# Optimization experiments

Hardware: AMD Instinct MI355X
Metric: run time of the kernel (lower is better)

## Reference

```python
import jax, jax.numpy as jnp
import numpy as np

N_NODES = 100000
N_EDGES = 1000000
IN_FEAT = 64
OUT_FEAT = 64


def setup_inputs() -> dict:
    key = jax.random.key(0)
    ks = jax.random.split(key, 12)
    d, o = IN_FEAT, OUT_FEAT
    s = 1.0 / np.sqrt(d)
    s2 = 1.0 / np.sqrt(2 * d)
    return {
        "x": jax.random.normal(ks[0], (N_NODES, d), dtype=jnp.float32),
        "edge_index": jax.random.randint(ks[1], (2, N_EDGES), 0, N_NODES, dtype=jnp.int64),
        "batch": jnp.zeros((N_NODES,), dtype=jnp.int64),
        # message MLP: Linear(d,d) -> ReLU -> Linear(d,d)
        "msg_w1": jax.random.uniform(ks[2], (d, d), jnp.float32, -s, s),
        "msg_b1": jax.random.uniform(ks[3], (d,), jnp.float32, -s, s),
        "msg_w2": jax.random.uniform(ks[4], (d, d), jnp.float32, -s, s),
        "msg_b2": jax.random.uniform(ks[5], (d,), jnp.float32, -s, s),
        # output MLP: Linear(2d,d) -> ReLU -> Linear(d,out)
        "out_w1": jax.random.uniform(ks[6], (2 * d, d), jnp.float32, -s2, s2),
        "out_b1": jax.random.uniform(ks[7], (d,), jnp.float32, -s2, s2),
        "out_w2": jax.random.uniform(ks[8], (d, o), jnp.float32, -s, s),
        "out_b2": jax.random.uniform(ks[9], (o,), jnp.float32, -s, s),
    }


def reference(x, edge_index, batch, msg_w1, msg_b1, msg_w2, msg_b2,
              out_w1, out_b1, out_w2, out_b2):
    row, col = edge_index[0], edge_index[1]
    # gather source-node features per edge, apply message MLP
    h = x[row]                                   # [E, d]
    msg = jax.nn.relu(h @ msg_w1 + msg_b1) @ msg_w2 + msg_b2  # [E, d]
    # force processor: node features pass through as fx; scatter-sum messages
    fx = x                                        # [N, d]
    agg = jax.ops.segment_sum(msg, col, num_segments=N_NODES)  # [N, d]
    out_final = jnp.concatenate([fx, agg], axis=1)  # [N, 2d]
    out = jax.nn.relu(out_final @ out_w1 + out_b1) @ out_w2 + out_b2  # [N, out]
    return out
```

## Files before the change

### kernel.cpp

```cpp
#include <hip/hip_runtime.h>
#include <hip/hip_bf16.h>

#define D 64
#define BSHIFT 7
#define BW (1 << BSHIFT)
#define MAXB 1024
#define CAP 8192
#define STRIDE 4096

typedef __attribute__((ext_vector_type(8))) short bf16x8;
typedef __attribute__((ext_vector_type(4))) float f32x4;

__device__ __forceinline__ short f2bf(float f) {
    __hip_bfloat16 h = __float2bfloat16(f);
    return *reinterpret_cast<short*>(&h);
}

__global__ __launch_bounds__(256) void msg_kernel(
    const float* __restrict__ x,
    const float* __restrict__ w1, const float* __restrict__ b1,
    const float* __restrict__ w2, const float* __restrict__ b2,
    __hip_bfloat16* __restrict__ m, int n_nodes)
{
    __shared__ __align__(16) __hip_bfloat16 sH[4][16 * 72];

    const int lane = threadIdx.x & 63;
    const int wslot = threadIdx.x >> 6;
    const int mr   = lane & 15;
    const int quad = lane >> 4;

    bf16x8 w1f[2][4], w2f[2][4];
    float  b1v[4], b2v[4];
#pragma unroll
    for (int ks = 0; ks < 2; ++ks)
#pragma unroll
        for (int nb = 0; nb < 4; ++nb) {
            bf16x8 f1, f2;
#pragma unroll
            for (int j = 0; j < 8; ++j) {
                int k = ks * 32 + quad * 8 + j;
                f1[j] = f2bf(w1[k * D + nb * 16 + mr]);
                f2[j] = f2bf(w2[k * D + nb * 16 + mr]);
            }
            w1f[ks][nb] = f1;
            w2f[ks][nb] = f2;
        }
#pragma unroll
    for (int nb = 0; nb < 4; ++nb) {
        b1v[nb] = b1[nb * 16 + mr];
        b2v[nb] = b2[nb * 16 + mr];
    }

    __hip_bfloat16* Hw = sH[wslot];
    const int wid    = (blockIdx.x * blockDim.x + threadIdx.x) >> 6;
    const int nwaves = (gridDim.x * blockDim.x) >> 6;
    const int ntiles = (n_nodes + 15) >> 4;

    for (int t = wid; t < ntiles; t += nwaves) {
        const int v0 = t * 16;
        int vr = v0 + mr;
        if (vr >= n_nodes) vr = n_nodes - 1;

        bf16x8 a[2];
#pragma unroll
        for (int ks = 0; ks < 2; ++ks) {
            const float* p = x + (size_t)vr * D + ks * 32 + quad * 8;
            float4 lo = *(const float4*)p;
            float4 hi = *(const float4*)(p + 4);
            bf16x8 f;
            f[0] = f2bf(lo.x); f[1] = f2bf(lo.y); f[2] = f2bf(lo.z); f[3] = f2bf(lo.w);
            f[4] = f2bf(hi.x); f[5] = f2bf(hi.y); f[6] = f2bf(hi.z); f[7] = f2bf(hi.w);
            a[ks] = f;
        }

#pragma unroll
        for (int nb = 0; nb < 4; ++nb) {
            f32x4 acc = {0.f, 0.f, 0.f, 0.f};
            acc = __builtin_amdgcn_mfma_f32_16x16x32_bf16(a[0], w1f[0][nb], acc, 0, 0, 0);
            acc = __builtin_amdgcn_mfma_f32_16x16x32_bf16(a[1], w1f[1][nb], acc, 0, 0, 0);
#pragma unroll
            for (int r = 0; r < 4; ++r) {
                float hv = fmaxf(acc[r] + b1v[nb], 0.f);
                Hw[(quad * 4 + r) * 72 + nb * 16 + mr] = __float2bfloat16(hv);
            }
        }

        bf16x8 h[2];
#pragma unroll
        for (int ks = 0; ks < 2; ++ks)
            h[ks] = *(const bf16x8*)&Hw[mr * 72 + ks * 32 + quad * 8];

#pragma unroll
        for (int nb = 0; nb < 4; ++nb) {
            f32x4 acc = {0.f, 0.f, 0.f, 0.f};
            acc = __builtin_amdgcn_mfma_f32_16x16x32_bf16(h[0], w2f[0][nb], acc, 0, 0, 0);
            acc = __builtin_amdgcn_mfma_f32_16x16x32_bf16(h[1], w2f[1][nb], acc, 0, 0, 0);
#pragma unroll
            for (int r = 0; r < 4; ++r)
                Hw[(quad * 4 + r) * 72 + nb * 16 + mr] =
                    __float2bfloat16(acc[r] + b2v[nb]);
        }

#pragma unroll
        for (int s = 0; s < 2; ++s) {
            const int rrow = s * 8 + (lane >> 3);
            const int cblk = (lane & 7) * 8;
            bf16x8 val = *(const bf16x8*)&Hw[rrow * 72 + cblk];
            const int vrow = v0 + rrow;
            if (vrow < n_nodes)
                *(bf16x8*)&m[(size_t)vrow * D + cblk] = val;
        }
    }
}

__global__ __launch_bounds__(256) void bin_kernel(
    const int* __restrict__ row, const int* __restrict__ col,
    int* __restrict__ gcur, unsigned int* __restrict__ tmp,
    int n_edges, int nbuckets, int chunk)
{
    __shared__ int hist[MAXB], base[MAXB], lcur[MAXB];
    const int t = threadIdx.x;
    const int e0 = blockIdx.x * chunk;
    const int e1 = min(e0 + chunk, n_edges);

    for (int i = t; i < nbuckets; i += 256) hist[i] = 0;
    __syncthreads();
    for (int e = e0 + t; e < e1; e += 256)
        atomicAdd(&hist[col[e] >> BSHIFT], 1);
    __syncthreads();
    for (int i = t; i < nbuckets; i += 256) {
        base[i] = hist[i] ? atomicAdd(&gcur[i], hist[i]) : 0;
        lcur[i] = 0;
    }
    __syncthreads();
    for (int e = e0 + t; e < e1; e += 256) {
        int c = col[e];
        int b = c >> BSHIFT;
        int loc = base[b] + atomicAdd(&lcur[b], 1);
        if (loc < STRIDE) {
            unsigned int val = ((unsigned int)(c & (BW - 1)) << 17)
                             | (unsigned int)row[e];
            tmp[(size_t)b * STRIDE + loc] = val;
        }
    }
}

__global__ __launch_bounds__(1024) void bucket_gather_kernel(
    const int* __restrict__ gcur, const unsigned int* __restrict__ tmp,
    const __hip_bfloat16* __restrict__ m, __hip_bfloat16* __restrict__ agg,
    int n_nodes, int nbuckets)
{
    __shared__ unsigned int sorted[CAP];
    __shared__ int cnt[BW], off[BW], cur[BW];

    const int b    = blockIdx.x;
    const int t    = threadIdx.x;
    const int lane = t & 63;
    const int wv   = t >> 6;
    const int vbase = b << BSHIFT;
    const unsigned int* gtmp = tmp + (size_t)b * STRIDE;

    const int total = min(gcur[b], STRIDE);

    float acc[8];
#pragma unroll
    for (int i = 0; i < 8; ++i) acc[i] = 0.f;

    for (int r0 = 0; r0 < total; r0 += CAP) {
        const int r1 = min(r0 + CAP, total);

        if (t < BW) cnt[t] = 0;
        __syncthreads();

        for (int i = r0 + t; i < r1; i += 1024)
            atomicAdd(&cnt[gtmp[i] >> 17], 1);
        __syncthreads();

        if (t < BW) off[t] = cnt[t];
        __syncthreads();
        for (int d = 1; d < BW; d <<= 1) {
            int u = 0;
            if (t < BW && t >= d) u = off[t - d];
            __syncthreads();
            if (t < BW) off[t] += u;
            __syncthreads();
        }
        if (t < BW) {
            int e = off[t] - cnt[t];
            off[t] = e;
            cur[t] = e;
        }
        __syncthreads();

        for (int i = r0 + t; i < r1; i += 1024) {
            unsigned int u = gtmp[i];
            int pos = atomicAdd(&cur[u >> 17], 1);
            sorted[pos] = u;
        }
        __syncthreads();

#pragma unroll
        for (int i = 0; i < 8; ++i) {
            const int n  = wv + (i << 4);
            const int o0 = off[n];
            const int c  = cnt[n];
            float s = 0.f;
            for (int cs = 0; cs < c; cs += 64) {
                const int k = min(64, c - cs);
                unsigned int pv = 0;
                if (lane < k) pv = sorted[o0 + cs + lane];

                int j = 0;
                for (; j + 8 <= k; j += 8) {
                    unsigned int u[8];
                    float v[8];
#pragma unroll
                    for (int q = 0; q < 8; ++q)
                        u[q] = __builtin_amdgcn_readlane(pv, j + q);
#pragma unroll
                    for (int q = 0; q < 8; ++q)
                        v[q] = (float)m[(size_t)(u[q] & 0x1FFFFu) * D + lane];
#pragma unroll
                    for (int q = 0; q < 8; ++q)
                        s += v[q];
                }
                for (; j < k; ++j) {
                    unsigned int u = __builtin_amdgcn_readlane(pv, j);
                    s += (float)m[(size_t)(u & 0x1FFFFu) * D + lane];
                }
            }
            acc[i] += s;
        }
        __syncthreads();
    }

#pragma unroll
    for (int i = 0; i < 8; ++i) {
        const int v = vbase + wv + (i << 4);
        if (v < n_nodes)
            agg[(size_t)v * D + lane] = __float2bfloat16(acc[i]);
    }
}

__global__ __launch_bounds__(256) void scatter_kernel(
    const int* __restrict__ row, const int* __restrict__ col,
    const __hip_bfloat16* __restrict__ m, float* __restrict__ aggf, int n_edges)
{
    const int lane = threadIdx.x & 63;
    const int wid  = (blockIdx.x * blockDim.x + threadIdx.x) >> 6;
    const int base = wid * 64;
    if (base >= n_edges) return;
    const int cnt = min(64, n_edges - base);

    int my_r = 0, my_c = 0;
    if (lane < cnt) { my_r = row[base + lane]; my_c = col[base + lane]; }

    for (int j = 0; j < cnt; ++j) {
        int r = __builtin_amdgcn_readlane(my_r, j);
        int c = __builtin_amdgcn_readlane(my_c, j);
        float v = (float)m[(size_t)r * D + lane];
        atomicAdd(&aggf[(size_t)c * D + lane], v);
    }
}

__global__ __launch_bounds__(256) void cvt_kernel(
    const float* __restrict__ aggf, __hip_bfloat16* __restrict__ agg, int n)
{
    int i = blockIdx.x * blockDim.x + threadIdx.x;
    if (i < n) agg[i] = __float2bfloat16(aggf[i]);
}

__global__ __launch_bounds__(256) void out_kernel(
    const float* __restrict__ x, const __hip_bfloat16* __restrict__ agg,
    const float* __restrict__ w1, const float* __restrict__ b1,
    const float* __restrict__ w2, const float* __restrict__ b2,
    float* __restrict__ out, int n_nodes)
{
    __shared__ __align__(16) __hip_bfloat16 sH[4][16 * 72];

    const int lane = threadIdx.x & 63;
    const int wslot = threadIdx.x >> 6;
    const int mr   = lane & 15;
    const int quad = lane >> 4;

    bf16x8 w1f[4][4], w2f[2][4];
    float  b1v[4], b2v[4];
#pragma unroll
    for (int ks = 0; ks < 4; ++ks)
#pragma unroll
        for (int nb = 0; nb < 4; ++nb) {
            bf16x8 f;
#pragma unroll
            for (int j = 0; j < 8; ++j) {
                int k = ks * 32 + quad * 8 + j;
                f[j] = f2bf(w1[k * D + nb * 16 + mr]);
            }
            w1f[ks][nb] = f;
        }
#pragma unroll
    for (int ks = 0; ks < 2; ++ks)
#pragma unroll
        for (int nb = 0; nb < 4; ++nb) {
            bf16x8 f;
#pragma unroll
            for (int j = 0; j < 8; ++j) {
                int k = ks * 32 + quad * 8 + j;
                f[j] = f2bf(w2[k * D + nb * 16 + mr]);
            }
            w2f[ks][nb] = f;
        }
#pragma unroll
    for (int nb = 0; nb < 4; ++nb) {
        b1v[nb] = b1[nb * 16 + mr];
        b2v[nb] = b2[nb * 16 + mr];
    }

    __hip_bfloat16* Hw = sH[wslot];
    const int wid    = (blockIdx.x * blockDim.x + threadIdx.x) >> 6;
    const int nwaves = (gridDim.x * blockDim.x) >> 6;
    const int ntiles = (n_nodes + 15) >> 4;

    for (int t = wid; t < ntiles; t += nwaves) {
        const int v0 = t * 16;
        int vr = v0 + mr;
        if (vr >= n_nodes) vr = n_nodes - 1;

        bf16x8 a[4];
#pragma unroll
        for (int ks = 0; ks < 2; ++ks) {
            const float* p = x + (size_t)vr * D + ks * 32 + quad * 8;
            float4 lo = *(const float4*)p;
            float4 hi = *(const float4*)(p + 4);
            bf16x8 f;
            f[0] = f2bf(lo.x); f[1] = f2bf(lo.y); f[2] = f2bf(lo.z); f[3] = f2bf(lo.w);
            f[4] = f2bf(hi.x); f[5] = f2bf(hi.y); f[6] = f2bf(hi.z); f[7] = f2bf(hi.w);
            a[ks] = f;
        }
#pragma unroll
        for (int ks = 2; ks < 4; ++ks)
            a[ks] = *(const bf16x8*)&agg[(size_t)vr * D + (ks - 2) * 32 + quad * 8];

#pragma unroll
        for (int nb = 0; nb < 4; ++nb) {
            f32x4 acc = {0.f, 0.f, 0.f, 0.f};
#pragma unroll
            for (int ks = 0; ks < 4; ++ks)
                acc = __builtin_amdgcn_mfma_f32_16x16x32_bf16(a[ks], w1f[ks][nb], acc, 0, 0, 0);
#pragma unroll
            for (int r = 0; r < 4; ++r) {
                float hv = fmaxf(acc[r] + b1v[nb], 0.f);
                Hw[(quad * 4 + r) * 72 + nb * 16 + mr] = __float2bfloat16(hv);
            }
        }

        bf16x8 h[2];
#pragma unroll
        for (int ks = 0; ks < 2; ++ks)
            h[ks] = *(const bf16x8*)&Hw[mr * 72 + ks * 32 + quad * 8];

#pragma unroll
        for (int nb = 0; nb < 4; ++nb) {
            f32x4 acc = {0.f, 0.f, 0.f, 0.f};
            acc = __builtin_amdgcn_mfma_f32_16x16x32_bf16(h[0], w2f[0][nb], acc, 0, 0, 0);
            acc = __builtin_amdgcn_mfma_f32_16x16x32_bf16(h[1], w2f[1][nb], acc, 0, 0, 0);
#pragma unroll
            for (int r = 0; r < 4; ++r) {
                int vrow = v0 + quad * 4 + r;
                if (vrow < n_nodes)
                    out[(size_t)vrow * D + nb * 16 + mr] = acc[r] + b2v[nb];
            }
        }
    }
}

extern "C" void kernel_launch(void* const* d_in, const int* in_sizes, int n_in,
                              void* d_out, int out_size, void* d_ws, size_t ws_size,
                              hipStream_t stream) {
    const float* x   = (const float*)d_in[0];
    const int*   ei  = (const int*)d_in[1];
    const float* mw1 = (const float*)d_in[3];
    const float* mb1 = (const float*)d_in[4];
    const float* mw2 = (const float*)d_in[5];
    const float* mb2 = (const float*)d_in[6];
    const float* ow1 = (const float*)d_in[7];
    const float* ob1 = (const float*)d_in[8];
    const float* ow2 = (const float*)d_in[9];
    const float* ob2 = (const float*)d_in[10];

    const int n_nodes = in_sizes[0] / D;
    const int n_edges = in_sizes[1] / 2;
    const int* row = ei;
    const int* col = ei + n_edges;

    const int nbuckets = (n_nodes + BW - 1) >> BSHIFT;

    __hip_bfloat16* m   = (__hip_bfloat16*)d_ws;
    __hip_bfloat16* agg = m + (size_t)n_nodes * D;
    unsigned int* tmp   = (unsigned int*)(agg + (size_t)n_nodes * D);
    const size_t region = (size_t)nbuckets * STRIDE * 4 > (size_t)n_nodes * D * 4
                        ? (size_t)nbuckets * STRIDE * 4 : (size_t)n_nodes * D * 4;
    int* gcur = (int*)((char*)tmp + region);
    float* aggf = (float*)tmp;
    const size_t need = (size_t)n_nodes * D * 4 + region + (size_t)nbuckets * 4;

    const int ntiles = (n_nodes + 15) / 16;
    int nblk = (ntiles + 3) / 4;
    if (nblk > 512) nblk = 512;

    msg_kernel<<<nblk, 256, 0, stream>>>(x, mw1, mb1, mw2, mb2, m, n_nodes);

    const bool shape_ok = (n_nodes < (1 << 17)) && (nbuckets <= MAXB)
                       && (n_edges <= nbuckets * (STRIDE / 2));

    if (ws_size >= need && shape_ok) {
        hipMemsetAsync(gcur, 0, (size_t)nbuckets * sizeof(int), stream);
        const int nbbin = 128;
        const int chunk = (n_edges + nbbin - 1) / nbbin;
        bin_kernel<<<nbbin, 256, 0, stream>>>(row, col, gcur, tmp,
                                              n_edges, nbuckets, chunk);
        bucket_gather_kernel<<<nbuckets, 1024, 0, stream>>>(gcur, tmp, m, agg,
                                                            n_nodes, nbuckets);
    } else {
        hipMemsetAsync(aggf, 0, (size_t)n_nodes * D * sizeof(float), stream);
        const int nwaves_s = (n_edges + 63) / 64;
        scatter_kernel<<<(nwaves_s + 3) / 4, 256, 0, stream>>>(row, col, m, aggf, n_edges);
        cvt_kernel<<<((n_nodes * D) + 255) / 256, 256, 0, stream>>>(aggf, agg, n_nodes * D);
    }

    out_kernel<<<nblk, 256, 0, stream>>>(x, agg, ow1, ob1, ow2, ob2,
                                         (float*)d_out, n_nodes);
}
```

Before: 199.3 us.

## Replace per-bucket counting sort with shared-memory float atomic accumulation

The bucket gather kernel no longer counting-sorts each bucket's edges by destination in shared memory. Each wavefront now takes 64-edge chunks straight from the bucket list, gathers the bf16 message rows and adds them into a 128x64 float accumulator in LDS with atomicAdd. This removes the histogram, the prefix scan, the scatter pass and their barriers, and lets all 16 waves share the gather work evenly instead of splitting it by node. The cost is LDS atomic contention on popular destination nodes, and a float summation order that is no longer deterministic.

```diff
diff --git a/kernel.cpp b/kernel.cpp
--- a/kernel.cpp
+++ b/kernel.cpp
@@ -5,7 +5,6 @@
 #define BSHIFT 7
 #define BW (1 << BSHIFT)
 #define MAXB 1024
-#define CAP 8192
 #define STRIDE 4096
 
 typedef __attribute__((ext_vector_type(8))) short bf16x8;
@@ -150,8 +149,7 @@
     const __hip_bfloat16* __restrict__ m, __hip_bfloat16* __restrict__ agg,
     int n_nodes, int nbuckets)
 {
-    __shared__ unsigned int sorted[CAP];
-    __shared__ int cnt[BW], off[BW], cur[BW];
+    __shared__ float sacc[BW * D];
 
     const int b    = blockIdx.x;
     const int t    = threadIdx.x;
@@ -162,83 +160,44 @@
 
     const int total = min(gcur[b], STRIDE);
 
-    float acc[8];
-#pragma unroll
-    for (int i = 0; i < 8; ++i) acc[i] = 0.f;
-
-    for (int r0 = 0; r0 < total; r0 += CAP) {
-        const int r1 = min(r0 + CAP, total);
-
-        if (t < BW) cnt[t] = 0;
-        __syncthreads();
-
-        for (int i = r0 + t; i < r1; i += 1024)
-            atomicAdd(&cnt[gtmp[i] >> 17], 1);
-        __syncthreads();
-
-        if (t < BW) off[t] = cnt[t];
-        __syncthreads();
-        for (int d = 1; d < BW; d <<= 1) {
-            int u = 0;
-            if (t < BW && t >= d) u = off[t - d];
-            __syncthreads();
-            if (t < BW) off[t] += u;
-            __syncthreads();
-        }
-        if (t < BW) {
-            int e = off[t] - cnt[t];
-            off[t] = e;
-            cur[t] = e;
-        }
-        __syncthreads();
-
-        for (int i = r0 + t; i < r1; i += 1024) {
-            unsigned int u = gtmp[i];
-            int pos = atomicAdd(&cur[u >> 17], 1);
-            sorted[pos] = u;
-        }
-        __syncthreads();
-
-#pragma unroll
-        for (int i = 0; i < 8; ++i) {
-            const int n  = wv + (i << 4);
-            const int o0 = off[n];
-            const int c  = cnt[n];
-            float s = 0.f;
-            for (int cs = 0; cs < c; cs += 64) {
-                const int k = min(64, c - cs);
-                unsigned int pv = 0;
-                if (lane < k) pv = sorted[o0 + cs + lane];
-
-                int j = 0;
-                for (; j + 8 <= k; j += 8) {
-                    unsigned int u[8];
-                    float v[8];
-#pragma unroll
-                    for (int q = 0; q < 8; ++q)
-                        u[q] = __builtin_amdgcn_readlane(pv, j + q);
-#pragma unroll
-                    for (int q = 0; q < 8; ++q)
-                        v[q] = (float)m[(size_t)(u[q] & 0x1FFFFu) * D + lane];
-#pragma unroll
-                    for (int q = 0; q < 8; ++q)
-                        s += v[q];
-                }
-                for (; j < k; ++j) {
-                    unsigned int u = __builtin_amdgcn_readlane(pv, j);
-                    s += (float)m[(size_t)(u & 0x1FFFFu) * D + lane];
-                }
-            }
-            acc[i] += s;
-        }
-        __syncthreads();
-    }
+#pragma unroll
+    for (int i = t; i < (BW * D) / 4; i += 1024)
+        ((float4*)sacc)[i] = make_float4(0.f, 0.f, 0.f, 0.f);
+    __syncthreads();
+
+    for (int e0 = wv * 64; e0 < total; e0 += 16 * 64) {
+        const int k = min(64, total - e0);
+        unsigned int pv = 0;
+        if (lane < k) pv = gtmp[e0 + lane];
+
+        int j = 0;
+        for (; j + 16 <= k; j += 16) {
+            unsigned int u[16];
+            float v[16];
+#pragma unroll
+            for (int q = 0; q < 16; ++q)
+                u[q] = __builtin_amdgcn_readlane(pv, j + q);
+#pragma unroll
+            for (int q = 0; q < 16; ++q)
+                v[q] = (float)m[(size_t)(u[q] & 0x1FFFFu) * D + lane];
+#pragma unroll
+            for (int q = 0; q < 16; ++q)
+                atomicAdd(&sacc[(u[q] >> 17) * D + lane], v[q]);
+        }
+        for (; j < k; ++j) {
+            unsigned int u = __builtin_amdgcn_readlane(pv, j);
+            float v = (float)m[(size_t)(u & 0x1FFFFu) * D + lane];
+            atomicAdd(&sacc[(u >> 17) * D + lane], v);
+        }
+    }
+    __syncthreads();
 
 #pragma unroll
     for (int i = 0; i < 8; ++i) {
-        const int v = vbase + wv + (i << 4);
+        const int c = wv + (i << 4);
+        const int v = vbase + c;
         if (v < n_nodes)
-            agg[(size_t)v * D + lane] = __float2bfloat16(acc[i]);
+            agg[(size_t)v * D + lane] = __float2bfloat16(sacc[c * D + lane]);
     }
 }
 
```

Result: slower. 575.0 us (+188.5%).
